# Performance work log

Measured on AMD Instinct MI355X. Metric: run time of the kernel, lower is better.

The kernel has to match this reference:

```python
import jax, jax.numpy as jnp
import numpy as np

B, H, W, C = 32, 256, 256, 3
FLAT = (H // 4) * (W // 4) * 64  # 64*64*64 = 262144 after two stride-2 SAME convs


def _conv(x, k, b, stride):
    y = jax.lax.conv_general_dilated(
        x, k, (stride, stride), 'SAME',
        dimension_numbers=('NHWC', 'HWIO', 'NHWC'))
    return jax.nn.relu(y + b)


def _grid_sample(img, theta):
    # STN: build normalized affine grid from theta [B,2,3], bilinear sample with
    # zero padding for out-of-bounds (GridSampler2D semantics).
    b, h, w, c = img.shape
    xs = (2.0 * jnp.arange(w, dtype=img.dtype) + 1.0) / w - 1.0
    ys = (2.0 * jnp.arange(h, dtype=img.dtype) + 1.0) / h - 1.0
    X, Y = jnp.meshgrid(xs, ys)                      # [H,W]
    base = jnp.stack([X, Y, jnp.ones_like(X)], -1)   # [H,W,3]
    g = jnp.einsum('bij,hwj->bhwi', theta, base)     # [B,H,W,2] (x,y) in [-1,1]
    px = (g[..., 0] + 1.0) * 0.5 * w - 0.5
    py = (g[..., 1] + 1.0) * 0.5 * h - 0.5
    x0 = jnp.floor(px); y0 = jnp.floor(py)
    wx1 = px - x0; wx0 = 1.0 - wx1
    wy1 = py - y0; wy0 = 1.0 - wy1

    bidx = jnp.arange(b)[:, None, None]

    def gather(yi, xi):
        valid = (xi >= 0) & (xi < w) & (yi >= 0) & (yi < h)
        xc = jnp.clip(xi, 0, w - 1).astype(jnp.int32)
        yc = jnp.clip(yi, 0, h - 1).astype(jnp.int32)
        v = img[bidx, yc, xc]                        # [B,H,W,C]
        return v * valid[..., None].astype(img.dtype)

    out = (gather(y0, x0) * (wy0 * wx0)[..., None]
           + gather(y0, x0 + 1) * (wy0 * wx1)[..., None]
           + gather(y0 + 1, x0) * (wy1 * wx0)[..., None]
           + gather(y0 + 1, x0 + 1) * (wy1 * wx1)[..., None])
    return out


def setup_inputs() -> dict:
    key = jax.random.key(0)
    ks = jax.random.split(key, 9)
    s = 0.05
    return {
        'inputs': jax.random.uniform(ks[0], (B, H, W, C), jnp.float32),
        'k1': jax.random.normal(ks[1], (3, 3, C, 32), jnp.float32) * s,
        'b1': jnp.zeros((32,), jnp.float32),
        'k2': jax.random.normal(ks[2], (3, 3, 32, 64), jnp.float32) * s,
        'b2': jnp.zeros((64,), jnp.float32),
        'w1': jax.random.normal(ks[3], (FLAT, 128), jnp.float32) * 0.002,
        'd1': jnp.zeros((128,), jnp.float32),
        'w2': jax.random.normal(ks[4], (128, 6), jnp.float32) * s,
        'd2': jnp.asarray([1, 0, 0, 0, 1, 0], jnp.float32),  # identity-ish bias
    }


def reference(inputs, k1, b1, k2, b2, w1, d1, w2, d2):
    x = _conv(inputs, k1, b1, 2)          # [B,H/2,W/2,32]
    x = _conv(x, k2, b2, 2)               # [B,H/4,W/4,64]
    x = x.reshape(x.shape[0], -1)         # [B,FLAT]
    x = jax.nn.relu(x @ w1 + d1)          # [B,128]
    theta = (x @ w2 + d2).reshape(-1, 2, 3)
    return _grid_sample(inputs, theta)
```

## Files before the change

kernel.cpp:

```cpp
#include <hip/hip_runtime.h>

#define IN_H 256
#define IN_W 256
#define C0   3
#define C1   32
#define H1   128
#define C2   64
#define H2   64
#define NB   32
#define K_FLAT (H2*H2*C2)
#define NHID 128

#define A1_IDX(b,p,y,ci,x2) ((((((size_t)(b)*2 + (p))*H1 + (y))*C1 + (ci))*64) + (x2))

__global__ __launch_bounds__(256)
void conv1_k(const float* __restrict__ in, const float* __restrict__ k1,
             const float* __restrict__ b1, float* __restrict__ a1p) {
  const int tid = threadIdx.x;
  const int ox  = tid & 127;
  const int cg  = __builtin_amdgcn_readfirstlane((tid >> 7) * 16);
  const int oy  = blockIdx.x;
  const int b   = blockIdx.y;

  float acc[16];
#pragma unroll
  for (int co = 0; co < 16; ++co) acc[co] = b1[cg + co];

#pragma unroll
  for (int dy = 0; dy < 3; ++dy) {
    const int iy  = 2*oy + dy;
    if (iy >= IN_H) continue;
#pragma unroll
    for (int dx = 0; dx < 3; ++dx) {
      const int ix  = 2*ox + dx;
      const bool ok = ix < IN_W;
      const int ixc = ok ? ix : (IN_W-1);
      const float* ip = in + ((size_t)(b*IN_H + iy)*IN_W + ixc)*C0;
      const float m  = ok ? 1.f : 0.f;
      const float v0 = ip[0] * m;
      const float v1 = ip[1] * m;
      const float v2 = ip[2] * m;
      const float* wp = k1 + (size_t)((dy*3+dx)*C0)*C1 + cg;
#pragma unroll
      for (int co = 0; co < 16; ++co)
        acc[co] = fmaf(v0, wp[co],
                  fmaf(v1, wp[C1+co],
                  fmaf(v2, wp[2*C1+co], acc[co])));
    }
  }
  const int p  = ox & 1;
  const int x2 = ox >> 1;
#pragma unroll
  for (int co = 0; co < 16; ++co)
    a1p[A1_IDX(b, p, oy, cg + co, x2)] = fmaxf(acc[co], 0.f);
}

__global__ __launch_bounds__(256)
void conv2_k(const float* __restrict__ a1p, const float* __restrict__ k2,
             const float* __restrict__ b2, float* __restrict__ a2) {
  const int tid = threadIdx.x;
  const int ox  = tid & 63;
  const int cg16 = __builtin_amdgcn_readfirstlane((tid >> 6) * 16);
  const int oy  = blockIdx.x;
  const int b   = blockIdx.y;

  float acc[16];
#pragma unroll
  for (int co = 0; co < 16; ++co) acc[co] = b2[cg16 + co];

  const float xm = (ox == 63) ? 0.f : 1.f;

#pragma unroll
  for (int dy = 0; dy < 3; ++dy) {
    const int iy = 2*oy + dy;
    if (iy >= H1) continue;
    const float* r0 = a1p + A1_IDX(b, 0, iy, 0, 0) + ox;
    const float* r1 = a1p + A1_IDX(b, 1, iy, 0, 0) + ox;
    const float* wp = k2 + (size_t)(dy*3*C1)*C2 + cg16;
#pragma unroll 4
    for (int ci = 0; ci < C1; ++ci) {
      const float v0 = r0[(size_t)ci*64];
      const float v1 = r1[(size_t)ci*64];
      const float v2 = r0[(size_t)ci*64 + 1] * xm;
      const float* w0 = wp + (size_t)ci*C2;
      const float* w1r = wp + (size_t)(C1 + ci)*C2;
      const float* w2r = wp + (size_t)(2*C1 + ci)*C2;
#pragma unroll
      for (int co = 0; co < 16; ++co)
        acc[co] = fmaf(v0, w0[co],
                  fmaf(v1, w1r[co],
                  fmaf(v2, w2r[co], acc[co])));
    }
  }
  float* op = a2 + ((size_t)(b*H2 + oy)*H2 + ox)*C2 + cg16;
#pragma unroll
  for (int g = 0; g < 4; ++g) {
    float4 o;
    o.x = fmaxf(acc[4*g+0], 0.f);
    o.y = fmaxf(acc[4*g+1], 0.f);
    o.z = fmaxf(acc[4*g+2], 0.f);
    o.w = fmaxf(acc[4*g+3], 0.f);
    ((float4*)op)[g] = o;
  }
}

#define FC1_G   1024
#define KSPAN   (K_FLAT / FC1_G)

__global__ __launch_bounds__(256)
void fc1_partial_k(const float* __restrict__ a2, const float* __restrict__ w1,
                   float* __restrict__ partial) {
  __shared__ __align__(16) float xT[KSPAN*36];
  const int tid = threadIdx.x;
  const int q   = tid & 31;
  const int bo  = tid >> 5;
  const int k0  = blockIdx.x * KSPAN;

  {
    const int lb  = tid >> 3;
    const int lkq = tid & 7;
#pragma unroll
    for (int j = 0; j < 8; ++j) {
      const int k4 = lkq*4 + j*32;
      float4 t = *(const float4*)(a2 + (size_t)lb*K_FLAT + k0 + k4);
      xT[(k4+0)*36 + lb] = t.x;
      xT[(k4+1)*36 + lb] = t.y;
      xT[(k4+2)*36 + lb] = t.z;
      xT[(k4+3)*36 + lb] = t.w;
    }
  }
  __syncthreads();

  float4 a0 = make_float4(0.f,0.f,0.f,0.f), a1v = a0, a2v = a0, a3v = a0;
#pragma unroll 8
  for (int k = 0; k < KSPAN; ++k) {
    const float4 w4 = *(const float4*)(w1 + (size_t)(k0 + k)*NHID + 4*q);
    const float4 xb = *(const float4*)&xT[k*36 + 4*bo];
    a0.x = fmaf(xb.x, w4.x, a0.x); a0.y = fmaf(xb.x, w4.y, a0.y);
    a0.z = fmaf(xb.x, w4.z, a0.z); a0.w = fmaf(xb.x, w4.w, a0.w);
    a1v.x = fmaf(xb.y, w4.x, a1v.x); a1v.y = fmaf(xb.y, w4.y, a1v.y);
    a1v.z = fmaf(xb.y, w4.z, a1v.z); a1v.w = fmaf(xb.y, w4.w, a1v.w);
    a2v.x = fmaf(xb.z, w4.x, a2v.x); a2v.y = fmaf(xb.z, w4.y, a2v.y);
    a2v.z = fmaf(xb.z, w4.z, a2v.z); a2v.w = fmaf(xb.z, w4.w, a2v.w);
    a3v.x = fmaf(xb.w, w4.x, a3v.x); a3v.y = fmaf(xb.w, w4.y, a3v.y);
    a3v.z = fmaf(xb.w, w4.z, a3v.z); a3v.w = fmaf(xb.w, w4.w, a3v.w);
  }

  float* pp = partial + (size_t)blockIdx.x*(NB*NHID) + 4*q;
  *(float4*)(pp + (4*bo+0)*NHID) = a0;
  *(float4*)(pp + (4*bo+1)*NHID) = a1v;
  *(float4*)(pp + (4*bo+2)*NHID) = a2v;
  *(float4*)(pp + (4*bo+3)*NHID) = a3v;
}

__global__ __launch_bounds__(128)
void fc1_reduce1_k(const float* __restrict__ partial, float* __restrict__ partial2) {
  const int t  = blockIdx.x*128 + threadIdx.x;
  const int gc = blockIdx.y;
  float s = 0.f;
#pragma unroll 8
  for (int g = gc*128; g < gc*128+128; ++g) s += partial[(size_t)g*(NB*NHID) + t];
  partial2[(size_t)gc*(NB*NHID) + t] = s;
}

__global__ __launch_bounds__(256)
void fc1_reduce2_k(const float* __restrict__ partial2, const float* __restrict__ d1,
                   float* __restrict__ h) {
  const int t = blockIdx.x*256 + threadIdx.x;
  float s = 0.f;
#pragma unroll
  for (int gc = 0; gc < 8; ++gc) s += partial2[(size_t)gc*(NB*NHID) + t];
  h[t] = fmaxf(s + d1[t & (NHID-1)], 0.f);
}

__global__ __launch_bounds__(192)
void theta_k(const float* __restrict__ h, const float* __restrict__ w2,
             const float* __restrict__ d2, float* __restrict__ theta) {
  const int t = threadIdx.x;
  if (t >= NB*6) return;
  const int b = t / 6, j = t % 6;
  float s0 = 0.f, s1 = 0.f, s2 = 0.f, s3 = 0.f;
  for (int n = 0; n < NHID; n += 4) {
    s0 = fmaf(h[b*NHID + n+0], w2[(n+0)*6 + j], s0);
    s1 = fmaf(h[b*NHID + n+1], w2[(n+1)*6 + j], s1);
    s2 = fmaf(h[b*NHID + n+2], w2[(n+2)*6 + j], s2);
    s3 = fmaf(h[b*NHID + n+3], w2[(n+3)*6 + j], s3);
  }
  theta[t] = (s0 + s1) + (s2 + s3) + d2[j];
}

__global__ __launch_bounds__(256)
void sample_k(const float* __restrict__ img, const float* __restrict__ theta,
              float* __restrict__ out) {
  const int x = threadIdx.x;
  const int y = blockIdx.x & (IN_H-1);
  const int b = blockIdx.x >> 8;
  const float* tp = theta + b*6;
  const float t0 = tp[0], t1 = tp[1], t2 = tp[2];
  const float t3 = tp[3], t4 = tp[4], t5 = tp[5];

  const float xs = (2.f*x + 1.f)*(1.f/IN_W) - 1.f;
  const float ys = (2.f*y + 1.f)*(1.f/IN_H) - 1.f;
  const float gx = fmaf(t0, xs, fmaf(t1, ys, t2));
  const float gy = fmaf(t3, xs, fmaf(t4, ys, t5));
  const float px = fmaf(gx + 1.f, 0.5f*IN_W, -0.5f);
  const float py = fmaf(gy + 1.f, 0.5f*IN_H, -0.5f);

  const float x0f = floorf(px), y0f = floorf(py);
  const int ix0 = (int)x0f, iy0 = (int)y0f;
  const float wx1 = px - x0f, wx0 = 1.f - wx1;
  const float wy1 = py - y0f, wy0 = 1.f - wy1;

  float r = 0.f, g = 0.f, bl = 0.f;
  const float* ib = img + (size_t)b*IN_H*IN_W*C0;

  auto tap = [&](int yi, int xi, float w) {
    const bool v = (xi >= 0) && (xi < IN_W) && (yi >= 0) && (yi < IN_H);
    const int xc = xi < 0 ? 0 : (xi > IN_W-1 ? IN_W-1 : xi);
    const int yc = yi < 0 ? 0 : (yi > IN_H-1 ? IN_H-1 : yi);
    const float* p = ib + ((size_t)yc*IN_W + xc)*C0;
    if (v) {
      r  = fmaf(w, p[0], r);
      g  = fmaf(w, p[1], g);
      bl = fmaf(w, p[2], bl);
    }
  };
  tap(iy0,   ix0,   wy0*wx0);
  tap(iy0,   ix0+1, wy0*wx1);
  tap(iy0+1, ix0,   wy1*wx0);
  tap(iy0+1, ix0+1, wy1*wx1);

  float* op = out + ((size_t)(b*IN_H + y)*IN_W + x)*C0;
  op[0] = r; op[1] = g; op[2] = bl;
}

extern "C" void kernel_launch(void* const* d_in, const int* in_sizes, int n_in,
                              void* d_out, int out_size, void* d_ws, size_t ws_size,
                              hipStream_t stream) {
  const float* in = (const float*)d_in[0];
  const float* k1 = (const float*)d_in[1];
  const float* b1 = (const float*)d_in[2];
  const float* k2 = (const float*)d_in[3];
  const float* b2 = (const float*)d_in[4];
  const float* w1 = (const float*)d_in[5];
  const float* d1 = (const float*)d_in[6];
  const float* w2 = (const float*)d_in[7];
  const float* d2 = (const float*)d_in[8];
  float* out = (float*)d_out;
  float* ws  = (float*)d_ws;

  float* a1p     = ws;
  float* a2      = ws + (size_t)16777216;
  float* partial = ws;
  float* part2   = ws + (size_t)4194304;
  float* h       = ws + (size_t)4227072;
  float* th      = ws + (size_t)4231168;

  hipLaunchKernelGGL(conv1_k,       dim3(128, 32), dim3(256), 0, stream, in, k1, b1, a1p);
  hipLaunchKernelGGL(conv2_k,       dim3(64, 32),  dim3(256), 0, stream, a1p, k2, b2, a2);
  hipLaunchKernelGGL(fc1_partial_k, dim3(FC1_G),   dim3(256), 0, stream, a2, w1, partial);
  hipLaunchKernelGGL(fc1_reduce1_k, dim3(32, 8),   dim3(128), 0, stream, partial, part2);
  hipLaunchKernelGGL(fc1_reduce2_k, dim3(16),      dim3(256), 0, stream, part2, d1, h);
  hipLaunchKernelGGL(theta_k,       dim3(1),       dim3(192), 0, stream, h, w2, d2, th);
  hipLaunchKernelGGL(sample_k,      dim3(NB*IN_H), dim3(256), 0, stream, in, th, out);
}
```

Measured before the change: 392.2 us.

## Register-block conv2 over two output columns and two rows per block

Each thread in conv2 now computes two adjacent output columns, so every weight read feeds two accumulator sets, and the input loads become float2 vectors shared between the two outputs. Each block covers two output rows, which halves the grid. A specialised edge path handles the last row block by clamping the row index and masking the values. This doubles accumulator registers and halves the number of blocks, which may reduce occupancy and parallelism.

```diff
diff --git a/kernel.cpp b/kernel.cpp
--- a/kernel.cpp
+++ b/kernel.cpp
@@ -55,52 +55,79 @@
     a1p[A1_IDX(b, p, oy, cg + co, x2)] = fmaxf(acc[co], 0.f);
 }
 
+#define CONV2_DY_LOOP(EDGE_)                                                   \
+  _Pragma("unroll")                                                            \
+  for (int dy = 0; dy < 3; ++dy) {                                             \
+    int iy = 2*oy + dy;                                                        \
+    float rm = 1.f;                                                            \
+    if (EDGE_) { if (iy >= H1) { iy = H1 - 1; rm = 0.f; } }                    \
+    const float* r0 = a1p + A1_IDX(b, 0, iy, 0, 0) + 2*lx;                     \
+    const float* r1 = a1p + A1_IDX(b, 1, iy, 0, 0) + 2*lx;                     \
+    const float* wp = k2 + (size_t)(dy*3*C1)*C2 + cg16;                        \
+    const float m2 = EDGE_ ? rm * xm : xm;                                     \
+    _Pragma("unroll 4")                                                        \
+    for (int ci = 0; ci < C1; ++ci) {                                          \
+      const float2 Av = *(const float2*)(r0 + (size_t)ci*64);                  \
+      const float  A2 = r0[(size_t)ci*64 + 2];                                 \
+      const float2 Bv = *(const float2*)(r1 + (size_t)ci*64);                  \
+      const float ax = EDGE_ ? Av.x*rm : Av.x;                                 \
+      const float ay = EDGE_ ? Av.y*rm : Av.y;                                 \
+      const float bx = EDGE_ ? Bv.x*rm : Bv.x;                                 \
+      const float by = EDGE_ ? Bv.y*rm : Bv.y;                                 \
+      const float a2v = A2 * m2;                                               \
+      const float* w0  = wp + (size_t)ci*C2;                                   \
+      const float* w1r = wp + (size_t)(C1 + ci)*C2;                            \
+      const float* w2r = wp + (size_t)(2*C1 + ci)*C2;                          \
+      _Pragma("unroll")                                                        \
+      for (int co = 0; co < 16; ++co) {                                        \
+        acc0[co] = fmaf(ax, w0[co],                                            \
+                   fmaf(bx, w1r[co],                                           \
+                   fmaf(ay,  w2r[co], acc0[co])));                             \
+        acc1[co] = fmaf(ay, w0[co],                                            \
+                   fmaf(by, w1r[co],                                           \
+                   fmaf(a2v, w2r[co], acc1[co])));                             \
+      }                                                                        \
+    }                                                                          \
+  }
+
 __global__ __launch_bounds__(256)
 void conv2_k(const float* __restrict__ a1p, const float* __restrict__ k2,
              const float* __restrict__ b2, float* __restrict__ a2) {
-  const int tid = threadIdx.x;
-  const int ox  = tid & 63;
+  const int tid  = threadIdx.x;
+  const int lane = tid & 63;
+  const int lx   = lane & 31;
+  const int oys  = lane >> 5;
   const int cg16 = __builtin_amdgcn_readfirstlane((tid >> 6) * 16);
-  const int oy  = blockIdx.x;
-  const int b   = blockIdx.y;
-
-  float acc[16];
-#pragma unroll
-  for (int co = 0; co < 16; ++co) acc[co] = b2[cg16 + co];
-
-  const float xm = (ox == 63) ? 0.f : 1.f;
-
-#pragma unroll
-  for (int dy = 0; dy < 3; ++dy) {
-    const int iy = 2*oy + dy;
-    if (iy >= H1) continue;
-    const float* r0 = a1p + A1_IDX(b, 0, iy, 0, 0) + ox;
-    const float* r1 = a1p + A1_IDX(b, 1, iy, 0, 0) + ox;
-    const float* wp = k2 + (size_t)(dy*3*C1)*C2 + cg16;
-#pragma unroll 4
-    for (int ci = 0; ci < C1; ++ci) {
-      const float v0 = r0[(size_t)ci*64];
-      const float v1 = r1[(size_t)ci*64];
-      const float v2 = r0[(size_t)ci*64 + 1] * xm;
-      const float* w0 = wp + (size_t)ci*C2;
-      const float* w1r = wp + (size_t)(C1 + ci)*C2;
-      const float* w2r = wp + (size_t)(2*C1 + ci)*C2;
-#pragma unroll
-      for (int co = 0; co < 16; ++co)
-        acc[co] = fmaf(v0, w0[co],
-                  fmaf(v1, w1r[co],
-                  fmaf(v2, w2r[co], acc[co])));
-    }
-  }
-  float* op = a2 + ((size_t)(b*H2 + oy)*H2 + ox)*C2 + cg16;
+  const int oy   = blockIdx.x * 2 + oys;
+  const int b    = blockIdx.y;
+
+  float acc0[16], acc1[16];
+#pragma unroll
+  for (int co = 0; co < 16; ++co) { acc0[co] = b2[cg16 + co]; acc1[co] = acc0[co]; }
+
+  const float xm = (lx == 31) ? 0.f : 1.f;
+
+  if (blockIdx.x == 31) {
+    CONV2_DY_LOOP(1)
+  } else {
+    CONV2_DY_LOOP(0)
+  }
+
+  float* op = a2 + ((size_t)((b*H2 + oy)*H2) + 2*lx)*C2 + cg16;
 #pragma unroll
   for (int g = 0; g < 4; ++g) {
-    float4 o;
-    o.x = fmaxf(acc[4*g+0], 0.f);
-    o.y = fmaxf(acc[4*g+1], 0.f);
-    o.z = fmaxf(acc[4*g+2], 0.f);
-    o.w = fmaxf(acc[4*g+3], 0.f);
-    ((float4*)op)[g] = o;
+    float4 o0;
+    o0.x = fmaxf(acc0[4*g+0], 0.f);
+    o0.y = fmaxf(acc0[4*g+1], 0.f);
+    o0.z = fmaxf(acc0[4*g+2], 0.f);
+    o0.w = fmaxf(acc0[4*g+3], 0.f);
+    ((float4*)op)[g] = o0;
+    float4 o1;
+    o1.x = fmaxf(acc1[4*g+0], 0.f);
+    o1.y = fmaxf(acc1[4*g+1], 0.f);
+    o1.z = fmaxf(acc1[4*g+2], 0.f);
+    o1.w = fmaxf(acc1[4*g+3], 0.f);
+    ((float4*)(op + C2))[g] = o1;
   }
 }
 
@@ -257,7 +284,7 @@
   float* th      = ws + (size_t)4231168;
 
   hipLaunchKernelGGL(conv1_k,       dim3(128, 32), dim3(256), 0, stream, in, k1, b1, a1p);
-  hipLaunchKernelGGL(conv2_k,       dim3(64, 32),  dim3(256), 0, stream, a1p, k2, b2, a2);
+  hipLaunchKernelGGL(conv2_k,       dim3(32, 32),  dim3(256), 0, stream, a1p, k2, b2, a2);
   hipLaunchKernelGGL(fc1_partial_k, dim3(FC1_G),   dim3(256), 0, stream, a2, w1, partial);
   hipLaunchKernelGGL(fc1_reduce1_k, dim3(32, 8),   dim3(128), 0, stream, partial, part2);
   hipLaunchKernelGGL(fc1_reduce2_k, dim3(16),      dim3(256), 0, stream, part2, d1, h);
```

New measurement: 372.2 us. 5.1% less time.
